# Kernel optimization log

Hardware: AMD Instinct MI355X
Metric: run time of the kernel (lower is better)

Reference implementation:

```python
import jax, jax.numpy as jnp
import numpy as np

N = 100000
E = 300000
D = 128
EPS = 1e-5


def sage_conv(x, edge_index, Wl, bl, Wr):
    # PyG SAGEConv: out = lin_l(mean_{j in N(i)} x_j) + lin_r(x_i)
    src, dst = edge_index[0], edge_index[1]
    n = x.shape[0]
    agg = jax.ops.segment_sum(x[src], dst, num_segments=n)            # [N, d]
    cnt = jax.ops.segment_sum(jnp.ones((src.shape[0],), x.dtype), dst, num_segments=n)
    mean = agg / jnp.maximum(cnt, 1.0)[:, None]
    return mean @ Wl.T + bl + x @ Wr.T


def setup_inputs() -> dict:
    key = jax.random.key(0)
    ks = jax.random.split(key, 16)
    s = 0.05
    inp = {
        "feat": jax.random.normal(ks[0], (N, D), jnp.float32),
        "e0": jax.random.randint(ks[1], (2, E), 0, N, jnp.int32),
        "e1": jax.random.randint(ks[2], (2, E), 0, N, jnp.int32),
        "e2": jax.random.randint(ks[3], (2, E), 0, N, jnp.int32),
    }
    # per-etype SAGEConv params (in=hidden=128)
    for i, k in zip(range(3), (ks[4], ks[5], ks[6])):
        ka, kb = jax.random.split(k)
        inp[f"Wl{i}"] = jax.random.normal(ka, (D, D), jnp.float32) * s
        inp[f"bl{i}"] = jnp.zeros((D,), jnp.float32)
        inp[f"Wr{i}"] = jax.random.normal(kb, (D, D), jnp.float32) * s
    ka, kb = jax.random.split(ks[7])
    inp["Wla"] = jax.random.normal(ka, (D, D), jnp.float32) * s
    inp["bla"] = jnp.zeros((D,), jnp.float32)
    inp["Wra"] = jax.random.normal(kb, (D, D), jnp.float32) * s
    ka, kb = jax.random.split(ks[8])
    inp["Wf"] = jax.random.normal(ka, (D, D), jnp.float32) * s
    inp["bf"] = jnp.zeros((D,), jnp.float32)
    inp["Wrf"] = jax.random.normal(kb, (D, D), jnp.float32) * s
    inp["gamma"] = jnp.ones((D,), jnp.float32)
    inp["beta"] = jnp.zeros((D,), jnp.float32)
    inp["wt"] = jnp.ones((3,), jnp.float32)
    return inp


def reference(feat, Wl0, bl0, Wr0, Wl1, bl1, Wr1, Wl2, bl2, Wr2,
              Wla, bla, Wra, Wf, bf, Wrf, gamma, beta, wt, e0, e1, e2):
    out0 = sage_conv(feat, e0, Wl0, bl0, Wr0)
    out1 = sage_conv(feat, e1, Wl1, bl1, Wr1)
    out2 = sage_conv(feat, e2, Wl2, bl2, Wr2)
    all_e = jnp.concatenate([e0, e1, e2], axis=1)   # [2, 3E]
    all_out = sage_conv(feat, all_e, Wla, bla, Wra)
    comb = wt[0] * out0 + wt[1] * out1 + wt[2] * out2 + all_out
    comb = jax.nn.relu(comb)
    # BatchNorm1d (training mode: batch stats over node dim, biased var)
    mu = jnp.mean(comb, axis=0)
    var = jnp.mean((comb - mu) ** 2, axis=0)
    comb = (comb - mu) * jax.lax.rsqrt(var + EPS) * gamma + beta
    # dropout p=0.0 -> identity
    return sage_conv(comb, all_e, Wf, bf, Wrf)
```

## Files before the change

### kernel.cpp

```cpp
#include <hip/hip_runtime.h>

#define NN 100000
#define NE 300000
#define DD 128
#define NBLKG 782
#define NBLKSEG 49

typedef short bf16x8 __attribute__((ext_vector_type(8)));
typedef float f32x4 __attribute__((ext_vector_type(4)));
typedef unsigned u32x4 __attribute__((ext_vector_type(4)));

__device__ __forceinline__ unsigned short f2b(float f) {
    union { float f; unsigned u; } c; c.f = f;
    unsigned u = c.u;
    return (unsigned short)((u + 0x7fffu + ((u >> 16) & 1u)) >> 16);
}
__device__ __forceinline__ float b2lo(unsigned u) {
    union { float f; unsigned u; } c; c.u = u << 16; return c.f;
}
__device__ __forceinline__ float b2hi(unsigned u) {
    union { float f; unsigned u; } c; c.u = u & 0xffff0000u; return c.f;
}
__device__ __forceinline__ unsigned pack2(float lo, float hi) {
    return (unsigned)f2b(lo) | ((unsigned)f2b(hi) << 16);
}

__global__ __launch_bounds__(256) void feat_to_bf16(
    const float* __restrict__ feat, unsigned short* __restrict__ fb) {
    int gid = blockIdx.x * 256 + threadIdx.x;
    if (gid >= NN * 16) return;
    const f32x4* f4 = (const f32x4*)feat;
    f32x4 a = __builtin_nontemporal_load(&f4[gid * 2]);
    f32x4 b = __builtin_nontemporal_load(&f4[gid * 2 + 1]);
    uint4 o;
    o.x = pack2(a.x, a.y); o.y = pack2(a.z, a.w);
    o.z = pack2(b.x, b.y); o.w = pack2(b.z, b.w);
    ((uint4*)fb)[gid] = o;
}

__global__ __launch_bounds__(256) void prep_weights(
    const float* __restrict__ Wl0, const float* __restrict__ bl0, const float* __restrict__ Wr0,
    const float* __restrict__ Wl1, const float* __restrict__ bl1, const float* __restrict__ Wr1,
    const float* __restrict__ Wl2, const float* __restrict__ bl2, const float* __restrict__ Wr2,
    const float* __restrict__ Wla, const float* __restrict__ bla, const float* __restrict__ Wra,
    const float* __restrict__ Wf,  const float* __restrict__ bfv, const float* __restrict__ Wrf,
    const float* __restrict__ wt,
    unsigned short* __restrict__ WcatB, float* __restrict__ bias1,
    unsigned short* __restrict__ W2catB, float* __restrict__ bias2) {
    int idx = blockIdx.x * 256 + threadIdx.x;
    float w0 = wt[0], w1 = wt[1], w2 = wt[2];
    if (idx < 81920) {
        int f = idx / 640, k = idx % 640;
        float v;
        if (k < 128)      v = w0 * Wl0[f * 128 + k];
        else if (k < 256) v = w1 * Wl1[f * 128 + (k - 128)];
        else if (k < 384) v = w2 * Wl2[f * 128 + (k - 256)];
        else if (k < 512) v = Wla[f * 128 + (k - 384)];
        else {
            int kk = k - 512;
            v = w0 * Wr0[f * 128 + kk] + w1 * Wr1[f * 128 + kk] +
                w2 * Wr2[f * 128 + kk] + Wra[f * 128 + kk];
        }
        WcatB[idx] = f2b(v);
    } else if (idx < 81920 + 32768) {
        int j = idx - 81920;
        int f = j >> 8, k = j & 255;
        W2catB[j] = f2b((k < 128) ? Wf[f * 128 + k] : Wrf[f * 128 + (k - 128)]);
    } else if (idx < 81920 + 32768 + 128) {
        int f = idx - (81920 + 32768);
        bias1[f] = w0 * bl0[f] + w1 * bl1[f] + w2 * bl2[f] + bla[f];
        bias2[f] = bfv[f];
    }
}

__global__ __launch_bounds__(256) void count_deg(
    const int* __restrict__ e0, const int* __restrict__ e1, const int* __restrict__ e2,
    int* __restrict__ deg) {
    int gid = blockIdx.x * 256 + threadIdx.x;
    if (gid >= 3 * NE) return;
    int t = (gid < NE) ? 0 : ((gid < 2 * NE) ? 1 : 2);
    int i = gid - t * NE;
    const int* ep = (t == 0) ? e0 : ((t == 1) ? e1 : e2);
    atomicAdd(&deg[t * NN + ep[NE + i]], 1);
}

__global__ __launch_bounds__(256) void scan_local(
    const int* __restrict__ deg, int* __restrict__ rowstart, int* __restrict__ bsum) {
    __shared__ int sc[256];
    int b = blockIdx.x, tid = threadIdx.x;
    int seg = b / NBLKSEG, blk = b % NBLKSEG;
    int g0 = seg * NN;
    int base = blk * 2048 + tid * 8;
    int vals[8]; int tsum = 0;
#pragma unroll
    for (int j = 0; j < 8; ++j) {
        int l = base + j;
        int d = (l < NN) ? deg[g0 + l] : 0;
        vals[j] = tsum; tsum += d;
    }
    sc[tid] = tsum;
    __syncthreads();
    for (int off = 1; off < 256; off <<= 1) {
        int v = (tid >= off) ? sc[tid - off] : 0;
        __syncthreads();
        sc[tid] += v;
        __syncthreads();
    }
    int excl = sc[tid] - tsum;
#pragma unroll
    for (int j = 0; j < 8; ++j) {
        int l = base + j;
        if (l < NN) rowstart[g0 + l] = excl + vals[j];
    }
    if (tid == 255) bsum[b] = sc[255];
}

__global__ void scan_bsum(int* __restrict__ bsum) {
    int tid = threadIdx.x;
    if (tid < 3) {
        int run = 0;
        for (int b = 0; b < NBLKSEG; ++b) {
            int idx = tid * NBLKSEG + b;
            int t = bsum[idx]; bsum[idx] = run; run += t;
        }
    }
}

__global__ __launch_bounds__(256) void scan_fix(
    int* __restrict__ rowstart, int* __restrict__ fillpos, const int* __restrict__ bsum) {
    int b = blockIdx.x, tid = threadIdx.x;
    int seg = b / NBLKSEG, blk = b % NBLKSEG;
    int g0 = seg * NN;
    int base = blk * 2048 + tid * 8;
    int off = bsum[b];
#pragma unroll
    for (int j = 0; j < 8; ++j) {
        int l = base + j;
        if (l < NN) {
            int r = rowstart[g0 + l] + off;
            rowstart[g0 + l] = r;
            fillpos[g0 + l] = r;
        }
    }
}

__global__ __launch_bounds__(256) void fill_csr(
    const int* __restrict__ e0, const int* __restrict__ e1, const int* __restrict__ e2,
    int* __restrict__ fillpos, int* __restrict__ csr) {
    int gid = blockIdx.x * 256 + threadIdx.x;
    if (gid >= 3 * NE) return;
    int t = (gid < NE) ? 0 : ((gid < 2 * NE) ? 1 : 2);
    int i = gid - t * NE;
    const int* ep = (t == 0) ? e0 : ((t == 1) ? e1 : e2);
    int src = ep[i], dst = ep[NE + i];
    int p = atomicAdd(&fillpos[t * NN + dst], 1);
    csr[t * NE + p] = src;
}

__global__ __launch_bounds__(256) void gather1(
    const unsigned short* __restrict__ featB,
    const int* __restrict__ deg, const int* __restrict__ rowstart, const int* __restrict__ csr,
    unsigned short* __restrict__ meanB) {
    int n = __builtin_amdgcn_readfirstlane((int)((blockIdx.x * 256 + threadIdx.x) >> 6));
    if (n >= NN) return;
    int lane = threadIdx.x & 63;
    int d0 = deg[n], d1 = deg[NN + n], d2 = deg[2 * NN + n];
    int r0 = rowstart[n], r1 = rowstart[NN + n], r2 = rowstart[2 * NN + n];
    int b1 = d0, b2 = d0 + d1, dall = b2 + d2;

    auto eidx = [&](int j) -> int {
        if (j < b1)      return r0 + j;
        else if (j < b2) return NE + r1 + (j - b1);
        else             return 2 * NE + r2 + (j - b2);
    };

    float p0 = 0.f, p1 = 0.f;
    float sA0 = 0.f, sA1 = 0.f;
    float sB0 = 0.f, sB1 = 0.f;

    unsigned f0 = 0, f1 = 0, f2 = 0;
    int i3 = 0;
    {
        int i0 = 0, i1 = 0, i2 = 0;
        if (dall > 0) i0 = csr[eidx(0)];
        if (dall > 1) i1 = csr[eidx(1)];
        if (dall > 2) i2 = csr[eidx(2)];
        if (dall > 3) i3 = csr[eidx(3)];
        if (dall > 0) f0 = *((const unsigned*)(featB + (size_t)i0 * DD) + lane);
        if (dall > 1) f1 = *((const unsigned*)(featB + (size_t)i1 * DD) + lane);
        if (dall > 2) f2 = *((const unsigned*)(featB + (size_t)i2 * DD) + lane);
    }
    for (int j = 0; j <= dall; ++j) {
        if (j == b1)   { sA0 = p0; sA1 = p1; }
        if (j == b2)   { sB0 = p0; sB1 = p1; }
        if (j == dall) break;
        unsigned u = f0;
        f0 = f1; f1 = f2;
        if (j + 3 < dall) f2 = *((const unsigned*)(featB + (size_t)i3 * DD) + lane);
        if (j + 4 < dall) i3 = csr[eidx(j + 4)];
        p0 += b2lo(u); p1 += b2hi(u);
    }

    float inv0 = 1.0f / fmaxf((float)d0, 1.0f);
    float inv1 = 1.0f / fmaxf((float)d1, 1.0f);
    float inv2 = 1.0f / fmaxf((float)d2, 1.0f);
    float inva = 1.0f / fmaxf((float)dall, 1.0f);
    float m10 = sB0 - sA0, m11 = sB1 - sA1;
    float m20 = p0 - sB0,  m21 = p1 - sB1;
    unsigned* outp = (unsigned*)(meanB + (size_t)n * 512) + lane;
    __builtin_nontemporal_store(pack2(sA0 * inv0, sA1 * inv0), outp);
    __builtin_nontemporal_store(pack2(m10 * inv1, m11 * inv1), outp + 64);
    __builtin_nontemporal_store(pack2(m20 * inv2, m21 * inv2), outp + 128);
    __builtin_nontemporal_store(pack2(p0 * inva,  p1 * inva),  outp + 192);
}

__global__ __launch_bounds__(256) void gemm1_tile(
    const unsigned short* __restrict__ meanB, const unsigned short* __restrict__ featB,
    const unsigned short* __restrict__ WcatB, const float* __restrict__ bias1,
    unsigned short* __restrict__ comb, float* __restrict__ partials) {
    __shared__ unsigned short ABs[65536 / 2];
    unsigned short* As = ABs;
    unsigned short* Bs = ABs + 16384;
    int tid = threadIdx.x;
    int wid = tid >> 6, lane = tid & 63;
    int quad = lane >> 4, m16 = lane & 15;
    int nb = blockIdx.x * 128;
    int mb = (wid & 1) * 64, fb = (wid >> 1) * 64;
    f32x4 acc[4][4];
#pragma unroll
    for (int mi = 0; mi < 4; ++mi)
#pragma unroll
        for (int fi = 0; fi < 4; ++fi) acc[mi][fi] = (f32x4){0.f, 0.f, 0.f, 0.f};

    for (int kc = 0; kc < 5; ++kc) {
        __syncthreads();
#pragma unroll
        for (int it = 0; it < 8; ++it) {
            int idx = it * 256 + tid;
            int row = idx >> 4, chunk = idx & 15;
            int s = chunk >> 2, q = chunk & 3;
            int gr = min(nb + row, NN - 1);
            u32x4 v = (kc < 4)
                ? __builtin_nontemporal_load((const u32x4*)(meanB + (size_t)gr * 512 + kc * 128 + chunk * 8))
                : *(const u32x4*)(featB + (size_t)gr * DD + chunk * 8);
            *(u32x4*)&As[(((s * 128 + row) * 4) + q) * 8] = v;
        }
#pragma unroll
        for (int it = 0; it < 8; ++it) {
            int idx = it * 256 + tid;
            int f = idx >> 4, chunk = idx & 15;
            int s = chunk >> 2, q = chunk & 3;
            u32x4 v = *(const u32x4*)(WcatB + (size_t)f * 640 + kc * 128 + chunk * 8);
            *(u32x4*)&Bs[(((s * 128 + f) * 4) + q) * 8] = v;
        }
        __syncthreads();
#pragma unroll
        for (int s = 0; s < 4; ++s) {
            bf16x8 av[4], bv[4];
#pragma unroll
            for (int mi = 0; mi < 4; ++mi)
                av[mi] = *(const bf16x8*)&As[(((s * 128 + mb + mi * 16 + m16) * 4) + quad) * 8];
#pragma unroll
            for (int fi = 0; fi < 4; ++fi)
                bv[fi] = *(const bf16x8*)&Bs[(((s * 128 + fb + fi * 16 + m16) * 4) + quad) * 8];
#pragma unroll
            for (int mi = 0; mi < 4; ++mi)
#pragma unroll
                for (int fi = 0; fi < 4; ++fi)
                    acc[mi][fi] = __builtin_amdgcn_mfma_f32_16x16x32_bf16(av[mi], bv[fi], acc[mi][fi], 0, 0, 0);
        }
    }
    __syncthreads();
    float* bnS = (float*)ABs;
    float* bnQ = bnS + 128;
    if (tid < 128) { bnS[tid] = 0.f; bnQ[tid] = 0.f; }
    __syncthreads();
#pragma unroll
    for (int fi = 0; fi < 4; ++fi) {
        int f = fb + fi * 16 + m16;
        float bb = bias1[f];
        float s = 0.f, q = 0.f;
#pragma unroll
        for (int mi = 0; mi < 4; ++mi) {
#pragma unroll
            for (int r = 0; r < 4; ++r) {
                int row = nb + mb + mi * 16 + quad * 4 + r;
                float v = fmaxf(acc[mi][fi][r] + bb, 0.f);
                if (row < NN) {
                    s += v; q += v * v;
                    comb[(size_t)row * DD + f] = f2b(v);
                }
            }
        }
        atomicAdd(&bnS[f], s);
        atomicAdd(&bnQ[f], q);
    }
    __syncthreads();
    if (tid < 128) {
        partials[(size_t)tid * NBLKG + blockIdx.x] = bnS[tid];
        partials[(size_t)(128 + tid) * NBLKG + blockIdx.x] = bnQ[tid];
    }
}

__global__ __launch_bounds__(256) void bnfin(
    const float* __restrict__ partials,
    const float* __restrict__ gamma, const float* __restrict__ beta,
    float* __restrict__ bnA, float* __restrict__ bnB) {
    __shared__ float rs[256], rq[256];
    int f = blockIdx.x, tid = threadIdx.x;
    float s = 0.f, q = 0.f;
    for (int r = tid; r < NBLKG; r += 256) {
        s += partials[(size_t)f * NBLKG + r];
        q += partials[(size_t)(128 + f) * NBLKG + r];
    }
    rs[tid] = s; rq[tid] = q;
    __syncthreads();
    for (int off = 128; off > 0; off >>= 1) {
        if (tid < off) { rs[tid] += rs[tid + off]; rq[tid] += rq[tid + off]; }
        __syncthreads();
    }
    if (tid == 0) {
        float mu = rs[0] / (float)NN;
        float var = fmaxf(rq[0] / (float)NN - mu * mu, 0.f);
        float a = gamma[f] * rsqrtf(var + 1e-5f);
        bnA[f] = a;
        bnB[f] = beta[f] - mu * a;
    }
}

__global__ __launch_bounds__(256) void gather2(
    const unsigned short* __restrict__ comb,
    const int* __restrict__ deg, const int* __restrict__ rowstart, const int* __restrict__ csr,
    const float* __restrict__ bnA, const float* __restrict__ bnB,
    unsigned short* __restrict__ meanC) {
    int n = __builtin_amdgcn_readfirstlane((int)((blockIdx.x * 256 + threadIdx.x) >> 6));
    if (n >= NN) return;
    int lane = threadIdx.x & 63;
    int d0 = deg[n], d1 = deg[NN + n], d2 = deg[2 * NN + n];
    int r0 = rowstart[n], r1 = rowstart[NN + n], r2 = rowstart[2 * NN + n];
    int b1 = d0, b2 = d0 + d1, dall = b2 + d2;

    auto eidx = [&](int j) -> int {
        if (j < b1)      return r0 + j;
        else if (j < b2) return NE + r1 + (j - b1);
        else             return 2 * NE + r2 + (j - b2);
    };

    float p0 = 0.f, p1 = 0.f;
    unsigned f0 = 0, f1 = 0, f2 = 0;
    int i3 = 0;
    {
        int i0 = 0, i1 = 0, i2 = 0;
        if (dall > 0) i0 = csr[eidx(0)];
        if (dall > 1) i1 = csr[eidx(1)];
        if (dall > 2) i2 = csr[eidx(2)];
        if (dall > 3) i3 = csr[eidx(3)];
        if (dall > 0) f0 = *((const unsigned*)(comb + (size_t)i0 * DD) + lane);
        if (dall > 1) f1 = *((const unsigned*)(comb + (size_t)i1 * DD) + lane);
        if (dall > 2) f2 = *((const unsigned*)(comb + (size_t)i2 * DD) + lane);
    }
    for (int j = 0; j < dall; ++j) {
        unsigned u = f0;
        f0 = f1; f1 = f2;
        if (j + 3 < dall) f2 = *((const unsigned*)(comb + (size_t)i3 * DD) + lane);
        if (j + 4 < dall) i3 = csr[eidx(j + 4)];
        p0 += b2lo(u); p1 += b2hi(u);
    }

    float v0 = 0.f, v1 = 0.f;
    if (dall > 0) {
        float inv = 1.0f / (float)dall;
        float2 a = *(const float2*)&bnA[lane * 2];
        float2 b = *(const float2*)&bnB[lane * 2];
        v0 = a.x * (p0 * inv) + b.x;
        v1 = a.y * (p1 * inv) + b.y;
    }
    __builtin_nontemporal_store(pack2(v0, v1),
                                (unsigned*)(meanC + (size_t)n * DD) + lane);
}

__global__ __launch_bounds__(256) void gemm2_tile(
    const unsigned short* __restrict__ meanC, const unsigned short* __restrict__ comb,
    const float* __restrict__ bnA, const float* __restrict__ bnB,
    const unsigned short* __restrict__ W2catB, const float* __restrict__ bias2,
    float* __restrict__ out) {
    __shared__ unsigned short ABs[65536 / 2];
    unsigned short* As = ABs;
    unsigned short* Bs = ABs + 16384;
    int tid = threadIdx.x;
    int wid = tid >> 6, lane = tid & 63;
    int quad = lane >> 4, m16 = lane & 15;
    int nb = blockIdx.x * 128;
    int mb = (wid & 1) * 64, fb = (wid >> 1) * 64;
    f32x4 acc[4][4];
#pragma unroll
    for (int mi = 0; mi < 4; ++mi)
#pragma unroll
        for (int fi = 0; fi < 4; ++fi) acc[mi][fi] = (f32x4){0.f, 0.f, 0.f, 0.f};

    for (int kc = 0; kc < 2; ++kc) {
        __syncthreads();
#pragma unroll
        for (int it = 0; it < 8; ++it) {
            int idx = it * 256 + tid;
            int row = idx >> 4, chunk = idx & 15;
            int s = chunk >> 2, q = chunk & 3;
            int gr = min(nb + row, NN - 1);
            u32x4 v;
            if (kc == 0) {
                v = __builtin_nontemporal_load((const u32x4*)(meanC + (size_t)gr * DD + chunk * 8));
            } else {
                u32x4 c4 = *(const u32x4*)(comb + (size_t)gr * DD + chunk * 8);
                int cb = chunk * 8;
                float4 a0 = *(const float4*)&bnA[cb], a1 = *(const float4*)&bnA[cb + 4];
                float4 b0 = *(const float4*)&bnB[cb], b1 = *(const float4*)&bnB[cb + 4];
                v.x = pack2(a0.x * b2lo(c4.x) + b0.x, a0.y * b2hi(c4.x) + b0.y);
                v.y = pack2(a0.z * b2lo(c4.y) + b0.z, a0.w * b2hi(c4.y) + b0.w);
                v.z = pack2(a1.x * b2lo(c4.z) + b1.x, a1.y * b2hi(c4.z) + b1.y);
                v.w = pack2(a1.z * b2lo(c4.w) + b1.z, a1.w * b2hi(c4.w) + b1.w);
            }
            *(u32x4*)&As[(((s * 128 + row) * 4) + q) * 8] = v;
        }
#pragma unroll
        for (int it = 0; it < 8; ++it) {
            int idx = it * 256 + tid;
            int f = idx >> 4, chunk = idx & 15;
            int s = chunk >> 2, q = chunk & 3;
            u32x4 v = *(const u32x4*)(W2catB + (size_t)f * 256 + kc * 128 + chunk * 8);
            *(u32x4*)&Bs[(((s * 128 + f) * 4) + q) * 8] = v;
        }
        __syncthreads();
#pragma unroll
        for (int s = 0; s < 4; ++s) {
            bf16x8 av[4], bv[4];
#pragma unroll
            for (int mi = 0; mi < 4; ++mi)
                av[mi] = *(const bf16x8*)&As[(((s * 128 + mb + mi * 16 + m16) * 4) + quad) * 8];
#pragma unroll
            for (int fi = 0; fi < 4; ++fi)
                bv[fi] = *(const bf16x8*)&Bs[(((s * 128 + fb + fi * 16 + m16) * 4) + quad) * 8];
#pragma unroll
            for (int mi = 0; mi < 4; ++mi)
#pragma unroll
                for (int fi = 0; fi < 4; ++fi)
                    acc[mi][fi] = __builtin_amdgcn_mfma_f32_16x16x32_bf16(av[mi], bv[fi], acc[mi][fi], 0, 0, 0);
        }
    }
#pragma unroll
    for (int fi = 0; fi < 4; ++fi) {
        int f = fb + fi * 16 + m16;
        float bb = bias2[f];
#pragma unroll
        for (int mi = 0; mi < 4; ++mi) {
#pragma unroll
            for (int r = 0; r < 4; ++r) {
                int row = nb + mb + mi * 16 + quad * 4 + r;
                if (row < NN)
                    __builtin_nontemporal_store(acc[mi][fi][r] + bb,
                                                &out[(size_t)row * DD + f]);
            }
        }
    }
}

extern "C" void kernel_launch(void* const* d_in, const int* in_sizes, int n_in,
                              void* d_out, int out_size, void* d_ws, size_t ws_size,
                              hipStream_t stream) {
    const float* feat = (const float*)d_in[0];
    const int* e0 = (const int*)d_in[1];
    const int* e1 = (const int*)d_in[2];
    const int* e2 = (const int*)d_in[3];
    const float* Wl0 = (const float*)d_in[4];
    const float* bl0 = (const float*)d_in[5];
    const float* Wr0 = (const float*)d_in[6];
    const float* Wl1 = (const float*)d_in[7];
    const float* bl1 = (const float*)d_in[8];
    const float* Wr1 = (const float*)d_in[9];
    const float* Wl2 = (const float*)d_in[10];
    const float* bl2 = (const float*)d_in[11];
    const float* Wr2 = (const float*)d_in[12];
    const float* Wla = (const float*)d_in[13];
    const float* bla = (const float*)d_in[14];
    const float* Wra = (const float*)d_in[15];
    const float* Wf  = (const float*)d_in[16];
    const float* bfv = (const float*)d_in[17];
    const float* Wrf = (const float*)d_in[18];
    const float* gamma = (const float*)d_in[19];
    const float* beta  = (const float*)d_in[20];
    const float* wt    = (const float*)d_in[21];

    int* deg      = (int*)d_ws;
    int* rowstart = deg + 3 * NN;
    int* fillpos  = rowstart + 3 * NN;
    int* csr      = fillpos + 3 * NN;
    int* bsum     = csr + 3 * NE;
    float* partials = (float*)(bsum + 160);
    float* bias1  = partials + 256 * NBLKG;
    float* bias2  = bias1 + 128;
    float* bnA    = bias2 + 128;
    float* bnB    = bnA + 128;
    unsigned short* WcatB  = (unsigned short*)(bnB + 128);
    unsigned short* W2catB = WcatB + 81920;
    unsigned short* comb   = W2catB + 32768;
    unsigned short* featB  = comb + (size_t)NN * DD;
    unsigned short* meanB  = featB + (size_t)NN * DD;
    unsigned short* meanC  = meanB + (size_t)NN * 512;

    hipMemsetAsync(deg, 0, (size_t)3 * NN * sizeof(int), stream);

    feat_to_bf16<<<6250, 256, 0, stream>>>(feat, featB);
    prep_weights<<<449, 256, 0, stream>>>(Wl0, bl0, Wr0, Wl1, bl1, Wr1, Wl2, bl2, Wr2,
                                          Wla, bla, Wra, Wf, bfv, Wrf, wt,
                                          WcatB, bias1, W2catB, bias2);
    count_deg<<<3516, 256, 0, stream>>>(e0, e1, e2, deg);
    scan_local<<<147, 256, 0, stream>>>(deg, rowstart, bsum);
    scan_bsum<<<1, 64, 0, stream>>>(bsum);
    scan_fix<<<147, 256, 0, stream>>>(rowstart, fillpos, bsum);
    fill_csr<<<3516, 256, 0, stream>>>(e0, e1, e2, fillpos, csr);

    gather1<<<25000, 256, 0, stream>>>(featB, deg, rowstart, csr, meanB);
    gemm1_tile<<<NBLKG, 256, 0, stream>>>(meanB, featB, WcatB, bias1, comb, partials);
    bnfin<<<128, 256, 0, stream>>>(partials, gamma, beta, bnA, bnB);
    gather2<<<25000, 256, 0, stream>>>(comb, deg, rowstart, csr, bnA, bnB, meanC);
    gemm2_tile<<<NBLKG, 256, 0, stream>>>(meanC, comb, bnA, bnB, W2catB, bias2,
                                          (float*)d_out);
}
```

Measured before the change: 463.7 us.

## Unify per-etype CSR into one interleaved CSR and fuse gather2 into gemm2

```diff
diff --git a/kernel.cpp b/kernel.cpp
--- a/kernel.cpp
+++ b/kernel.cpp
@@ -25,20 +25,11 @@
     return (unsigned)f2b(lo) | ((unsigned)f2b(hi) << 16);
 }
 
-__global__ __launch_bounds__(256) void feat_to_bf16(
-    const float* __restrict__ feat, unsigned short* __restrict__ fb) {
-    int gid = blockIdx.x * 256 + threadIdx.x;
-    if (gid >= NN * 16) return;
-    const f32x4* f4 = (const f32x4*)feat;
-    f32x4 a = __builtin_nontemporal_load(&f4[gid * 2]);
-    f32x4 b = __builtin_nontemporal_load(&f4[gid * 2 + 1]);
-    uint4 o;
-    o.x = pack2(a.x, a.y); o.y = pack2(a.z, a.w);
-    o.z = pack2(b.x, b.y); o.w = pack2(b.z, b.w);
-    ((uint4*)fb)[gid] = o;
-}
-
-__global__ __launch_bounds__(256) void prep_weights(
+#define NB_FEAT 6250
+#define NB_WT   449
+#define NB_DEG  3516
+__global__ __launch_bounds__(256) void prep_all(
+    const float* __restrict__ feat, unsigned short* __restrict__ fb,
     const float* __restrict__ Wl0, const float* __restrict__ bl0, const float* __restrict__ Wr0,
     const float* __restrict__ Wl1, const float* __restrict__ bl1, const float* __restrict__ Wr1,
     const float* __restrict__ Wl2, const float* __restrict__ bl2, const float* __restrict__ Wr2,
@@ -46,46 +37,57 @@
     const float* __restrict__ Wf,  const float* __restrict__ bfv, const float* __restrict__ Wrf,
     const float* __restrict__ wt,
     unsigned short* __restrict__ WcatB, float* __restrict__ bias1,
-    unsigned short* __restrict__ W2catB, float* __restrict__ bias2) {
-    int idx = blockIdx.x * 256 + threadIdx.x;
-    float w0 = wt[0], w1 = wt[1], w2 = wt[2];
-    if (idx < 81920) {
-        int f = idx / 640, k = idx % 640;
-        float v;
-        if (k < 128)      v = w0 * Wl0[f * 128 + k];
-        else if (k < 256) v = w1 * Wl1[f * 128 + (k - 128)];
-        else if (k < 384) v = w2 * Wl2[f * 128 + (k - 256)];
-        else if (k < 512) v = Wla[f * 128 + (k - 384)];
-        else {
-            int kk = k - 512;
-            v = w0 * Wr0[f * 128 + kk] + w1 * Wr1[f * 128 + kk] +
-                w2 * Wr2[f * 128 + kk] + Wra[f * 128 + kk];
-        }
-        WcatB[idx] = f2b(v);
-    } else if (idx < 81920 + 32768) {
-        int j = idx - 81920;
-        int f = j >> 8, k = j & 255;
-        W2catB[j] = f2b((k < 128) ? Wf[f * 128 + k] : Wrf[f * 128 + (k - 128)]);
-    } else if (idx < 81920 + 32768 + 128) {
-        int f = idx - (81920 + 32768);
-        bias1[f] = w0 * bl0[f] + w1 * bl1[f] + w2 * bl2[f] + bla[f];
-        bias2[f] = bfv[f];
-    }
-}
-
-__global__ __launch_bounds__(256) void count_deg(
+    unsigned short* __restrict__ W2catB, float* __restrict__ bias2,
     const int* __restrict__ e0, const int* __restrict__ e1, const int* __restrict__ e2,
     int* __restrict__ deg) {
-    int gid = blockIdx.x * 256 + threadIdx.x;
-    if (gid >= 3 * NE) return;
-    int t = (gid < NE) ? 0 : ((gid < 2 * NE) ? 1 : 2);
-    int i = gid - t * NE;
-    const int* ep = (t == 0) ? e0 : ((t == 1) ? e1 : e2);
-    atomicAdd(&deg[t * NN + ep[NE + i]], 1);
+    int b = blockIdx.x, tid = threadIdx.x;
+    if (b < NB_FEAT) {
+        int gid = b * 256 + tid;
+        if (gid >= NN * 16) return;
+        const f32x4* f4 = (const f32x4*)feat;
+        f32x4 a = __builtin_nontemporal_load(&f4[gid * 2]);
+        f32x4 c = __builtin_nontemporal_load(&f4[gid * 2 + 1]);
+        uint4 o;
+        o.x = pack2(a.x, a.y); o.y = pack2(a.z, a.w);
+        o.z = pack2(c.x, c.y); o.w = pack2(c.z, c.w);
+        ((uint4*)fb)[gid] = o;
+    } else if (b < NB_FEAT + NB_WT) {
+        int idx = (b - NB_FEAT) * 256 + tid;
+        float w0 = wt[0], w1 = wt[1], w2 = wt[2];
+        if (idx < 81920) {
+            int f = idx / 640, k = idx % 640;
+            float v;
+            if (k < 128)      v = w0 * Wl0[f * 128 + k];
+            else if (k < 256) v = w1 * Wl1[f * 128 + (k - 128)];
+            else if (k < 384) v = w2 * Wl2[f * 128 + (k - 256)];
+            else if (k < 512) v = Wla[f * 128 + (k - 384)];
+            else {
+                int kk = k - 512;
+                v = w0 * Wr0[f * 128 + kk] + w1 * Wr1[f * 128 + kk] +
+                    w2 * Wr2[f * 128 + kk] + Wra[f * 128 + kk];
+            }
+            WcatB[idx] = f2b(v);
+        } else if (idx < 81920 + 32768) {
+            int j = idx - 81920;
+            int f = j >> 8, k = j & 255;
+            W2catB[j] = f2b((k < 128) ? Wf[f * 128 + k] : Wrf[f * 128 + (k - 128)]);
+        } else if (idx < 81920 + 32768 + 128) {
+            int f = idx - (81920 + 32768);
+            bias1[f] = w0 * bl0[f] + w1 * bl1[f] + w2 * bl2[f] + bla[f];
+            bias2[f] = bfv[f];
+        }
+    } else {
+        int gid = (b - NB_FEAT - NB_WT) * 256 + tid;
+        if (gid >= 3 * NE) return;
+        int t = (gid < NE) ? 0 : ((gid < 2 * NE) ? 1 : 2);
+        int i = gid - t * NE;
+        const int* ep = (t == 0) ? e0 : ((t == 1) ? e1 : e2);
+        atomicAdd(&deg[t * NN + ep[NE + i]], 1);
+    }
 }
 
 __global__ __launch_bounds__(256) void scan_local(
-    const int* __restrict__ deg, int* __restrict__ rowstart, int* __restrict__ bsum) {
+    const int* __restrict__ deg, int* __restrict__ rsloc, int* __restrict__ bsum) {
     __shared__ int sc[256];
     int b = blockIdx.x, tid = threadIdx.x;
     int seg = b / NBLKSEG, blk = b % NBLKSEG;
@@ -110,7 +112,7 @@
 #pragma unroll
     for (int j = 0; j < 8; ++j) {
         int l = base + j;
-        if (l < NN) rowstart[g0 + l] = excl + vals[j];
+        if (l < NN) rsloc[g0 + l] = excl + vals[j];
     }
     if (tid == 255) bsum[b] = sc[255];
 }
@@ -127,26 +129,29 @@
 }
 
 __global__ __launch_bounds__(256) void scan_fix(
-    int* __restrict__ rowstart, int* __restrict__ fillpos, const int* __restrict__ bsum) {
-    int b = blockIdx.x, tid = threadIdx.x;
-    int seg = b / NBLKSEG, blk = b % NBLKSEG;
-    int g0 = seg * NN;
+    const int* __restrict__ deg, const int* __restrict__ rsloc, const int* __restrict__ bsum,
+    int* __restrict__ fillpos, int* __restrict__ rowstartU, int* __restrict__ degall) {
+    int blk = blockIdx.x, tid = threadIdx.x;
     int base = blk * 2048 + tid * 8;
-    int off = bsum[b];
+    int o0 = bsum[blk], o1 = bsum[NBLKSEG + blk], o2 = bsum[2 * NBLKSEG + blk];
 #pragma unroll
     for (int j = 0; j < 8; ++j) {
         int l = base + j;
         if (l < NN) {
-            int r = rowstart[g0 + l] + off;
-            rowstart[g0 + l] = r;
-            fillpos[g0 + l] = r;
+            int d0 = deg[l], d1 = deg[NN + l], d2 = deg[2 * NN + l];
+            int rU = (rsloc[l] + o0) + (rsloc[NN + l] + o1) + (rsloc[2 * NN + l] + o2);
+            fillpos[l] = rU;
+            fillpos[NN + l] = rU + d0;
+            fillpos[2 * NN + l] = rU + d0 + d1;
+            rowstartU[l] = rU;
+            degall[l] = d0 + d1 + d2;
         }
     }
 }
 
 __global__ __launch_bounds__(256) void fill_csr(
     const int* __restrict__ e0, const int* __restrict__ e1, const int* __restrict__ e2,
-    int* __restrict__ fillpos, int* __restrict__ csr) {
+    int* __restrict__ fillpos, int* __restrict__ csrU) {
     int gid = blockIdx.x * 256 + threadIdx.x;
     if (gid >= 3 * NE) return;
     int t = (gid < NE) ? 0 : ((gid < 2 * NE) ? 1 : 2);
@@ -154,53 +159,45 @@
     const int* ep = (t == 0) ? e0 : ((t == 1) ? e1 : e2);
     int src = ep[i], dst = ep[NE + i];
     int p = atomicAdd(&fillpos[t * NN + dst], 1);
-    csr[t * NE + p] = src;
+    csrU[p] = src;
 }
 
 __global__ __launch_bounds__(256) void gather1(
     const unsigned short* __restrict__ featB,
-    const int* __restrict__ deg, const int* __restrict__ rowstart, const int* __restrict__ csr,
+    const int* __restrict__ deg, const int* __restrict__ rowstartU,
+    const int* __restrict__ degall, const int* __restrict__ csrU,
     unsigned short* __restrict__ meanB) {
     int n = __builtin_amdgcn_readfirstlane((int)((blockIdx.x * 256 + threadIdx.x) >> 6));
     if (n >= NN) return;
     int lane = threadIdx.x & 63;
-    int d0 = deg[n], d1 = deg[NN + n], d2 = deg[2 * NN + n];
-    int r0 = rowstart[n], r1 = rowstart[NN + n], r2 = rowstart[2 * NN + n];
-    int b1 = d0, b2 = d0 + d1, dall = b2 + d2;
-
-    auto eidx = [&](int j) -> int {
-        if (j < b1)      return r0 + j;
-        else if (j < b2) return NE + r1 + (j - b1);
-        else             return 2 * NE + r2 + (j - b2);
-    };
+    int d0 = deg[n], d1 = deg[NN + n];
+    int dall = degall[n];
+    int b1 = d0, b2 = d0 + d1;
+    const int* cp = csrU + rowstartU[n];
 
     float p0 = 0.f, p1 = 0.f;
-    float sA0 = 0.f, sA1 = 0.f;
-    float sB0 = 0.f, sB1 = 0.f;
-
-    unsigned f0 = 0, f1 = 0, f2 = 0;
-    int i3 = 0;
-    {
-        int i0 = 0, i1 = 0, i2 = 0;
-        if (dall > 0) i0 = csr[eidx(0)];
-        if (dall > 1) i1 = csr[eidx(1)];
-        if (dall > 2) i2 = csr[eidx(2)];
-        if (dall > 3) i3 = csr[eidx(3)];
-        if (dall > 0) f0 = *((const unsigned*)(featB + (size_t)i0 * DD) + lane);
-        if (dall > 1) f1 = *((const unsigned*)(featB + (size_t)i1 * DD) + lane);
-        if (dall > 2) f2 = *((const unsigned*)(featB + (size_t)i2 * DD) + lane);
-    }
+    float sA0 = 0.f, sA1 = 0.f, sB0 = 0.f, sB1 = 0.f;
+    unsigned f0 = 0, f1 = 0, f2 = 0, f3 = 0;
+    int i4 = 0, i5 = 0;
+    if (dall > 0) f0 = *((const unsigned*)(featB + (size_t)cp[0] * DD) + lane);
+    if (dall > 1) f1 = *((const unsigned*)(featB + (size_t)cp[1] * DD) + lane);
+    if (dall > 2) f2 = *((const unsigned*)(featB + (size_t)cp[2] * DD) + lane);
+    if (dall > 3) f3 = *((const unsigned*)(featB + (size_t)cp[3] * DD) + lane);
+    if (dall > 4) i4 = cp[4];
+    if (dall > 5) i5 = cp[5];
     for (int j = 0; j <= dall; ++j) {
-        if (j == b1)   { sA0 = p0; sA1 = p1; }
-        if (j == b2)   { sB0 = p0; sB1 = p1; }
+        if (j == b1) { sA0 = p0; sA1 = p1; }
+        if (j == b2) { sB0 = p0; sB1 = p1; }
         if (j == dall) break;
         unsigned u = f0;
-        f0 = f1; f1 = f2;
-        if (j + 3 < dall) f2 = *((const unsigned*)(featB + (size_t)i3 * DD) + lane);
-        if (j + 4 < dall) i3 = csr[eidx(j + 4)];
+        f0 = f1; f1 = f2; f2 = f3;
+        if (j + 4 < dall) f3 = *((const unsigned*)(featB + (size_t)i4 * DD) + lane);
+        i4 = i5;
+        if (j + 6 < dall) i5 = cp[j + 6];
         p0 += b2lo(u); p1 += b2hi(u);
     }
 
+    int d2 = dall - b2;
     float inv0 = 1.0f / fmaxf((float)d0, 1.0f);
     float inv1 = 1.0f / fmaxf((float)d1, 1.0f);
     float inv2 = 1.0f / fmaxf((float)d2, 1.0f);
@@ -328,59 +325,10 @@
     }
 }
 
-__global__ __launch_bounds__(256) void gather2(
+__global__ __launch_bounds__(256, 2) void gemm2_fused(
     const unsigned short* __restrict__ comb,
-    const int* __restrict__ deg, const int* __restrict__ rowstart, const int* __restrict__ csr,
-    const float* __restrict__ bnA, const float* __restrict__ bnB,
-    unsigned short* __restrict__ meanC) {
-    int n = __builtin_amdgcn_readfirstlane((int)((blockIdx.x * 256 + threadIdx.x) >> 6));
-    if (n >= NN) return;
-    int lane = threadIdx.x & 63;
-    int d0 = deg[n], d1 = deg[NN + n], d2 = deg[2 * NN + n];
-    int r0 = rowstart[n], r1 = rowstart[NN + n], r2 = rowstart[2 * NN + n];
-    int b1 = d0, b2 = d0 + d1, dall = b2 + d2;
-
-    auto eidx = [&](int j) -> int {
-        if (j < b1)      return r0 + j;
-        else if (j < b2) return NE + r1 + (j - b1);
-        else             return 2 * NE + r2 + (j - b2);
-    };
-
-    float p0 = 0.f, p1 = 0.f;
-    unsigned f0 = 0, f1 = 0, f2 = 0;
-    int i3 = 0;
-    {
-        int i0 = 0, i1 = 0, i2 = 0;
-        if (dall > 0) i0 = csr[eidx(0)];
-        if (dall > 1) i1 = csr[eidx(1)];
-        if (dall > 2) i2 = csr[eidx(2)];
-        if (dall > 3) i3 = csr[eidx(3)];
-        if (dall > 0) f0 = *((const unsigned*)(comb + (size_t)i0 * DD) + lane);
-        if (dall > 1) f1 = *((const unsigned*)(comb + (size_t)i1 * DD) + lane);
-        if (dall > 2) f2 = *((const unsigned*)(comb + (size_t)i2 * DD) + lane);
-    }
-    for (int j = 0; j < dall; ++j) {
-        unsigned u = f0;
-        f0 = f1; f1 = f2;
-        if (j + 3 < dall) f2 = *((const unsigned*)(comb + (size_t)i3 * DD) + lane);
-        if (j + 4 < dall) i3 = csr[eidx(j + 4)];
-        p0 += b2lo(u); p1 += b2hi(u);
-    }
-
-    float v0 = 0.f, v1 = 0.f;
-    if (dall > 0) {
-        float inv = 1.0f / (float)dall;
-        float2 a = *(const float2*)&bnA[lane * 2];
-        float2 b = *(const float2*)&bnB[lane * 2];
-        v0 = a.x * (p0 * inv) + b.x;
-        v1 = a.y * (p1 * inv) + b.y;
-    }
-    __builtin_nontemporal_store(pack2(v0, v1),
-                                (unsigned*)(meanC + (size_t)n * DD) + lane);
-}
-
-__global__ __launch_bounds__(256) void gemm2_tile(
-    const unsigned short* __restrict__ meanC, const unsigned short* __restrict__ comb,
+    const int* __restrict__ rowstartU, const int* __restrict__ degall,
+    const int* __restrict__ csrU,
     const float* __restrict__ bnA, const float* __restrict__ bnB,
     const unsigned short* __restrict__ W2catB, const float* __restrict__ bias2,
     float* __restrict__ out) {
@@ -388,7 +336,8 @@
     unsigned short* As = ABs;
     unsigned short* Bs = ABs + 16384;
     int tid = threadIdx.x;
-    int wid = tid >> 6, lane = tid & 63;
+    int wid = __builtin_amdgcn_readfirstlane(tid >> 6);
+    int lane = tid & 63;
     int quad = lane >> 4, m16 = lane & 15;
     int nb = blockIdx.x * 128;
     int mb = (wid & 1) * 64, fb = (wid >> 1) * 64;
@@ -398,54 +347,112 @@
 #pragma unroll
         for (int fi = 0; fi < 4; ++fi) acc[mi][fi] = (f32x4){0.f, 0.f, 0.f, 0.f};
 
-    for (int kc = 0; kc < 2; ++kc) {
-        __syncthreads();
-#pragma unroll
-        for (int it = 0; it < 8; ++it) {
-            int idx = it * 256 + tid;
-            int row = idx >> 4, chunk = idx & 15;
-            int s = chunk >> 2, q = chunk & 3;
-            int gr = min(nb + row, NN - 1);
-            u32x4 v;
-            if (kc == 0) {
-                v = __builtin_nontemporal_load((const u32x4*)(meanC + (size_t)gr * DD + chunk * 8));
-            } else {
-                u32x4 c4 = *(const u32x4*)(comb + (size_t)gr * DD + chunk * 8);
-                int cb = chunk * 8;
-                float4 a0 = *(const float4*)&bnA[cb], a1 = *(const float4*)&bnA[cb + 4];
-                float4 b0 = *(const float4*)&bnB[cb], b1 = *(const float4*)&bnB[cb + 4];
-                v.x = pack2(a0.x * b2lo(c4.x) + b0.x, a0.y * b2hi(c4.x) + b0.y);
-                v.y = pack2(a0.z * b2lo(c4.y) + b0.z, a0.w * b2hi(c4.y) + b0.w);
-                v.z = pack2(a1.x * b2lo(c4.z) + b1.x, a1.y * b2hi(c4.z) + b1.y);
-                v.w = pack2(a1.z * b2lo(c4.w) + b1.z, a1.w * b2hi(c4.w) + b1.w);
+#pragma unroll
+    for (int it = 0; it < 8; ++it) {
+        int idx = it * 256 + tid;
+        int f = idx >> 4, chunk = idx & 15;
+        int s = chunk >> 2, q = chunk & 3;
+        u32x4 v = *(const u32x4*)(W2catB + (size_t)f * 256 + chunk * 8);
+        *(u32x4*)&Bs[(((s * 128 + f) * 4) + q) * 8] = v;
+    }
+
+    {
+        float2 a2 = *(const float2*)&bnA[lane * 2];
+        float2 bb2 = *(const float2*)&bnB[lane * 2];
+        int sA = lane >> 4, qA = (lane >> 2) & 3, eA = (lane & 3) * 2;
+        for (int k = 0; k < 32; ++k) {
+            int row = wid * 32 + k;
+            int n = min(nb + row, NN - 1);
+            const int* cp = csrU + rowstartU[n];
+            int dall = degall[n];
+            float p0 = 0.f, p1 = 0.f;
+            unsigned g0 = 0, g1 = 0, g2 = 0, g3 = 0;
+            int i4 = 0, i5 = 0;
+            if (dall > 0) g0 = *((const unsigned*)(comb + (size_t)cp[0] * DD) + lane);
+            if (dall > 1) g1 = *((const unsigned*)(comb + (size_t)cp[1] * DD) + lane);
+            if (dall > 2) g2 = *((const unsigned*)(comb + (size_t)cp[2] * DD) + lane);
+            if (dall > 3) g3 = *((const unsigned*)(comb + (size_t)cp[3] * DD) + lane);
+            if (dall > 4) i4 = cp[4];
+            if (dall > 5) i5 = cp[5];
+            for (int j = 0; j < dall; ++j) {
+                unsigned u = g0;
+                g0 = g1; g1 = g2; g2 = g3;
+                if (j + 4 < dall) g3 = *((const unsigned*)(comb + (size_t)i4 * DD) + lane);
+                i4 = i5;
+                if (j + 6 < dall) i5 = cp[j + 6];
+                p0 += b2lo(u); p1 += b2hi(u);
             }
-            *(u32x4*)&As[(((s * 128 + row) * 4) + q) * 8] = v;
-        }
-#pragma unroll
-        for (int it = 0; it < 8; ++it) {
-            int idx = it * 256 + tid;
-            int f = idx >> 4, chunk = idx & 15;
-            int s = chunk >> 2, q = chunk & 3;
-            u32x4 v = *(const u32x4*)(W2catB + (size_t)f * 256 + kc * 128 + chunk * 8);
-            *(u32x4*)&Bs[(((s * 128 + f) * 4) + q) * 8] = v;
-        }
-        __syncthreads();
-#pragma unroll
-        for (int s = 0; s < 4; ++s) {
-            bf16x8 av[4], bv[4];
-#pragma unroll
-            for (int mi = 0; mi < 4; ++mi)
-                av[mi] = *(const bf16x8*)&As[(((s * 128 + mb + mi * 16 + m16) * 4) + quad) * 8];
+            float v0 = 0.f, v1 = 0.f;
+            if (dall > 0) {
+                float inv = 1.0f / (float)dall;
+                v0 = a2.x * (p0 * inv) + bb2.x;
+                v1 = a2.y * (p1 * inv) + bb2.y;
+            }
+            *(unsigned*)&As[(((sA * 128 + row) * 4) + qA) * 8 + eA] = pack2(v0, v1);
+        }
+    }
+    __syncthreads();
+
+#pragma unroll
+    for (int s = 0; s < 4; ++s) {
+        bf16x8 av[4], bv[4];
+#pragma unroll
+        for (int mi = 0; mi < 4; ++mi)
+            av[mi] = *(const bf16x8*)&As[(((s * 128 + mb + mi * 16 + m16) * 4) + quad) * 8];
+#pragma unroll
+        for (int fi = 0; fi < 4; ++fi)
+            bv[fi] = *(const bf16x8*)&Bs[(((s * 128 + fb + fi * 16 + m16) * 4) + quad) * 8];
+#pragma unroll
+        for (int mi = 0; mi < 4; ++mi)
 #pragma unroll
             for (int fi = 0; fi < 4; ++fi)
-                bv[fi] = *(const bf16x8*)&Bs[(((s * 128 + fb + fi * 16 + m16) * 4) + quad) * 8];
-#pragma unroll
-            for (int mi = 0; mi < 4; ++mi)
-#pragma unroll
-                for (int fi = 0; fi < 4; ++fi)
-                    acc[mi][fi] = __builtin_amdgcn_mfma_f32_16x16x32_bf16(av[mi], bv[fi], acc[mi][fi], 0, 0, 0);
-        }
-    }
+                acc[mi][fi] = __builtin_amdgcn_mfma_f32_16x16x32_bf16(av[mi], bv[fi], acc[mi][fi], 0, 0, 0);
+    }
+    __syncthreads();
+
+#pragma unroll
+    for (int it = 0; it < 8; ++it) {
+        int idx = it * 256 + tid;
+        int row = idx >> 4, chunk = idx & 15;
+        int s = chunk >> 2, q = chunk & 3;
+        int gr = min(nb + row, NN - 1);
+        u32x4 c4 = *(const u32x4*)(comb + (size_t)gr * DD + chunk * 8);
+        int cb = chunk * 8;
+        float4 a0 = *(const float4*)&bnA[cb], a1 = *(const float4*)&bnA[cb + 4];
+        float4 b0 = *(const float4*)&bnB[cb], b1 = *(const float4*)&bnB[cb + 4];
+        u32x4 v;
+        v.x = pack2(a0.x * b2lo(c4.x) + b0.x, a0.y * b2hi(c4.x) + b0.y);
+        v.y = pack2(a0.z * b2lo(c4.y) + b0.z, a0.w * b2hi(c4.y) + b0.w);
+        v.z = pack2(a1.x * b2lo(c4.z) + b1.x, a1.y * b2hi(c4.z) + b1.y);
+        v.w = pack2(a1.z * b2lo(c4.w) + b1.z, a1.w * b2hi(c4.w) + b1.w);
+        *(u32x4*)&As[(((s * 128 + row) * 4) + q) * 8] = v;
+    }
+#pragma unroll
+    for (int it = 0; it < 8; ++it) {
+        int idx = it * 256 + tid;
+        int f = idx >> 4, chunk = idx & 15;
+        int s = chunk >> 2, q = chunk & 3;
+        u32x4 v = *(const u32x4*)(W2catB + (size_t)f * 256 + 128 + chunk * 8);
+        *(u32x4*)&Bs[(((s * 128 + f) * 4) + q) * 8] = v;
+    }
+    __syncthreads();
+
+#pragma unroll
+    for (int s = 0; s < 4; ++s) {
+        bf16x8 av[4], bv[4];
+#pragma unroll
+        for (int mi = 0; mi < 4; ++mi)
+            av[mi] = *(const bf16x8*)&As[(((s * 128 + mb + mi * 16 + m16) * 4) + quad) * 8];
+#pragma unroll
+        for (int fi = 0; fi < 4; ++fi)
+            bv[fi] = *(const bf16x8*)&Bs[(((s * 128 + fb + fi * 16 + m16) * 4) + quad) * 8];
+#pragma unroll
+        for (int mi = 0; mi < 4; ++mi)
+#pragma unroll
+            for (int fi = 0; fi < 4; ++fi)
+                acc[mi][fi] = __builtin_amdgcn_mfma_f32_16x16x32_bf16(av[mi], bv[fi], acc[mi][fi], 0, 0, 0);
+    }
+
 #pragma unroll
     for (int fi = 0; fi < 4; ++fi) {
         int f = fb + fi * 16 + m16;
@@ -490,11 +497,13 @@
     const float* wt    = (const float*)d_in[21];
 
     int* deg      = (int*)d_ws;
-    int* rowstart = deg + 3 * NN;
-    int* fillpos  = rowstart + 3 * NN;
-    int* csr      = fillpos + 3 * NN;
-    int* bsum     = csr + 3 * NE;
-    float* partials = (float*)(bsum + 160);
+    int* rsloc    = deg + 3 * NN;
+    int* fillpos  = rsloc + 3 * NN;
+    int* csrU     = fillpos + 3 * NN;
+    int* bsum     = csrU + 3 * NE;
+    int* rowstartU = bsum + 160;
+    int* degall    = rowstartU + NN;
+    float* partials = (float*)(degall + NN);
     float* bias1  = partials + 256 * NBLKG;
     float* bias2  = bias1 + 128;
     float* bnA    = bias2 + 128;
@@ -504,24 +513,23 @@
     unsigned short* comb   = W2catB + 32768;
     unsigned short* featB  = comb + (size_t)NN * DD;
     unsigned short* meanB  = featB + (size_t)NN * DD;
-    unsigned short* meanC  = meanB + (size_t)NN * 512;
 
     hipMemsetAsync(deg, 0, (size_t)3 * NN * sizeof(int), stream);
 
-    feat_to_bf16<<<6250, 256, 0, stream>>>(feat, featB);
-    prep_weights<<<449, 256, 0, stream>>>(Wl0, bl0, Wr0, Wl1, bl1, Wr1, Wl2, bl2, Wr2,
-                                          Wla, bla, Wra, Wf, bfv, Wrf, wt,
-                                          WcatB, bias1, W2catB, bias2);
-    count_deg<<<3516, 256, 0, stream>>>(e0, e1, e2, deg);
-    scan_local<<<147, 256, 0, stream>>>(deg, rowstart, bsum);
+    prep_all<<<NB_FEAT + NB_WT + NB_DEG, 256, 0, stream>>>(
+        feat, featB,
+        Wl0, bl0, Wr0, Wl1, bl1, Wr1, Wl2, bl2, Wr2,
+        Wla, bla, Wra, Wf, bfv, Wrf, wt,
+        WcatB, bias1, W2catB, bias2,
+        e0, e1, e2, deg);
+    scan_local<<<147, 256, 0, stream>>>(deg, rsloc, bsum);
     scan_bsum<<<1, 64, 0, stream>>>(bsum);
-    scan_fix<<<147, 256, 0, stream>>>(rowstart, fillpos, bsum);
-    fill_csr<<<3516, 256, 0, stream>>>(e0, e1, e2, fillpos, csr);
-
-    gather1<<<25000, 256, 0, stream>>>(featB, deg, rowstart, csr, meanB);
+    scan_fix<<<NBLKSEG, 256, 0, stream>>>(deg, rsloc, bsum, fillpos, rowstartU, degall);
+    fill_csr<<<3516, 256, 0, stream>>>(e0, e1, e2, fillpos, csrU);
+
+    gather1<<<25000, 256, 0, stream>>>(featB, deg, rowstartU, degall, csrU, meanB);
     gemm1_tile<<<NBLKG, 256, 0, stream>>>(meanB, featB, WcatB, bias1, comb, partials);
     bnfin<<<128, 256, 0, stream>>>(partials, gamma, beta, bnA, bnB);
-    gather2<<<25000, 256, 0, stream>>>(comb, deg, rowstart, csr, bnA, bnB, meanC);
-    gemm2_tile<<<NBLKG, 256, 0, stream>>>(meanC, comb, bnA, bnB, W2catB, bias2,
-                                          (float*)d_out);
-}
+    gemm2_fused<<<NBLKG, 256, 0, stream>>>(comb, rowstartU, degall, csrU,
+                                           bnA, bnB, W2catB, bias2, (float*)d_out);
+}
```

After: 557.6 us. 1.2x slower.
